# Kernel tuning notes

Measured on AMD Instinct MI355X. Metric: run time of the kernel, lower is better.

The kernel has to match this reference:

```python
import jax, jax.numpy as jnp
import numpy as np

B, N, M = 4, 512, 8192
QUERY_DIM, INPUT_DIM = 512, 256
HEADS, DIM_HEAD = 8, 64
ATT_DIM = HEADS * DIM_HEAD  # 512


def setup_inputs() -> dict:
    key = jax.random.key(0)
    ks = jax.random.split(key, 6)
    x = jax.random.normal(ks[0], (B, N, QUERY_DIM), dtype=jnp.float32)
    context = jax.random.normal(ks[1], (B, M, INPUT_DIM), dtype=jnp.float32)
    # Linear weights stored as [in, out] for x @ W
    Wq = jax.random.normal(ks[2], (QUERY_DIM, ATT_DIM), dtype=jnp.float32) / np.sqrt(QUERY_DIM)
    Wkv = jax.random.normal(ks[3], (INPUT_DIM, 2 * ATT_DIM), dtype=jnp.float32) / np.sqrt(INPUT_DIM)
    Wo = jax.random.normal(ks[4], (ATT_DIM, QUERY_DIM), dtype=jnp.float32) / np.sqrt(ATT_DIM)
    bo = jax.random.normal(ks[5], (QUERY_DIM,), dtype=jnp.float32) * 0.01
    return {"x": x, "context": context, "Wq": Wq, "Wkv": Wkv, "Wo": Wo, "bo": bo}


def reference(x, context, Wq, Wkv, Wo, bo):
    scale = DIM_HEAD ** -0.5
    q = x @ Wq                      # [B, N, H*D]
    kv = context @ Wkv              # [B, M, 2*H*D]
    k, v = jnp.split(kv, 2, axis=-1)
    # split heads: b n (h d) -> b h n d
    q = q.reshape(B, N, HEADS, DIM_HEAD).transpose(0, 2, 1, 3)
    k = k.reshape(B, M, HEADS, DIM_HEAD).transpose(0, 2, 1, 3)
    v = v.reshape(B, M, HEADS, DIM_HEAD).transpose(0, 2, 1, 3)
    scores = jnp.einsum('bhid,bhjd->bhij', q, k) * scale  # [B, H, N, M]
    attn = jax.nn.softmax(scores, axis=-1)
    out = jnp.einsum('bhij,bhjd->bhid', attn, v)           # [B, H, N, D]
    out = out.transpose(0, 2, 1, 3).reshape(B, N, ATT_DIM)
    return out @ Wo + bo
```

## Files before the change

### kernel.cpp

```cpp
#include <hip/hip_runtime.h>
#include <hip/hip_bf16.h>
#include <cstdint>

#define NB 4
#define NQ 512
#define NM 8192
#define NH 8
#define DH 64

typedef short bf16x8s __attribute__((ext_vector_type(8)));
typedef short bf16x4s __attribute__((ext_vector_type(4)));
typedef float f32x4  __attribute__((ext_vector_type(4)));

static __device__ __forceinline__ short f2bs(float f) {
    unsigned u = __builtin_bit_cast(unsigned, f);
    return (short)(unsigned short)((u + 0x8000u) >> 16);
}
static __device__ __forceinline__ unsigned pk2(float a, float b) {
    unsigned au = __builtin_bit_cast(unsigned, a) + 0x8000u;
    unsigned bu = __builtin_bit_cast(unsigned, b) + 0x8000u;
    return __builtin_amdgcn_perm(bu, au, 0x07060302u);
}

#if __has_builtin(__builtin_amdgcn_exp2f)
static __device__ __forceinline__ float fexp2(float x) { return __builtin_amdgcn_exp2f(x); }
#else
static __device__ __forceinline__ float fexp2(float x) { return exp2f(x); }
#endif

__global__ __launch_bounds__(256) void prep_weights(
    const float* __restrict__ Wq, const float* __restrict__ Wo,
    const float* __restrict__ Wkv,
    short* __restrict__ Wqf, short* __restrict__ Wof, short* __restrict__ Wkvf)
{
    const int t = threadIdx.x;
    const int w = t >> 6, ln = t & 63;
    const int m16 = ln & 15, quad = ln >> 4;
    int f = blockIdx.x * 4 + w;
    const float* src; short* dst; int N, KS, n0, ks;
    if (f < 512)       { src = Wq;  dst = Wqf;  N = 512;  KS = 16; n0 = f >> 4; ks = f & 15; }
    else if (f < 1024) { f -= 512;  src = Wo;  dst = Wof;  N = 512;  KS = 16; n0 = f >> 4; ks = f & 15; }
    else               { f -= 1024; src = Wkv; dst = Wkvf; N = 1024; KS = 8;  n0 = f >> 3; ks = f & 7; }
    const float* sp = src + (size_t)(ks * 32 + quad * 8) * N + n0 * 16 + m16;
    float v[8];
    #pragma unroll
    for (int j = 0; j < 8; ++j) v[j] = sp[(size_t)j * N];
    uint4 pkv = { pk2(v[0],v[1]), pk2(v[2],v[3]), pk2(v[4],v[5]), pk2(v[6],v[7]) };
    *(uint4*)(dst + ((size_t)(n0 * KS + ks) * 64 + ln) * 8) = pkv;
}

__device__ __forceinline__ void proj32_body(
    const float* __restrict__ A, const short* __restrict__ Wf,
    float* __restrict__ C, const float* __restrict__ bias,
    int tm, int tn, char* smemraw)
{
    short* As = (short*)smemraw;

    const int t = threadIdx.x;
    const int w = t >> 6, ln = t & 63;
    const int m16 = ln & 15, quad = ln >> 4;
    const int wm = w >> 1, wn = w & 1;

    const int ar = t >> 3, ac = (t & 7) << 3;

    const float* Ap = A + (size_t)(tm * 32 + ar) * 512 + ac;

    f32x4 acc[2] = {};

    for (int k0 = 0; k0 < 512; k0 += 64) {
        float4 a0 = *(const float4*)(Ap + k0);
        float4 a1 = *(const float4*)(Ap + k0 + 4);
        bf16x8s bfr[2][2];
        #pragma unroll
        for (int ks = 0; ks < 2; ++ks)
            #pragma unroll
            for (int nt = 0; nt < 2; ++nt)
                bfr[ks][nt] = *(const bf16x8s*)(Wf +
                    ((size_t)((tn * 4 + wn * 2 + nt) * 16 + (k0 >> 5) + ks) * 64 + ln) * 8);

        __syncthreads();
        {
            uint4 wa = { pk2(a0.x,a0.y), pk2(a0.z,a0.w), pk2(a1.x,a1.y), pk2(a1.z,a1.w) };
            *(uint4*)&As[ar * 72 + ac] = wa;
        }
        __syncthreads();

        #pragma unroll
        for (int ks = 0; ks < 2; ++ks) {
            bf16x8s af = *(const bf16x8s*)&As[(wm * 16 + m16) * 72 + ks * 32 + quad * 8];
            #pragma unroll
            for (int nt = 0; nt < 2; ++nt)
                acc[nt] = __builtin_amdgcn_mfma_f32_16x16x32_bf16(af, bfr[ks][nt], acc[nt], 0, 0, 0);
        }
    }

    const int row0 = tm * 32 + wm * 16 + quad * 4;
    const int col0 = tn * 64 + wn * 32;
    #pragma unroll
    for (int nt = 0; nt < 2; ++nt) {
        const int col = col0 + nt * 16 + m16;
        const float bb = bias ? bias[col] : 0.f;
        #pragma unroll
        for (int r = 0; r < 4; ++r)
            C[(size_t)(row0 + r) * 512 + col] = acc[nt][r] + bb;
    }
}

__device__ __forceinline__ void kv_body(
    const float* __restrict__ A, const short* __restrict__ Wkvf,
    short* __restrict__ Kf, short* __restrict__ Vf,
    int kvid, char* smemraw)
{
    short* As = (short*)smemraw;

    const int t  = threadIdx.x;
    const int tm = ((kvid >> 6) << 3) | (kvid & 7);
    const int tn = (kvid >> 3) & 7;
    const int w  = t >> 6, ln = t & 63;
    const int m16 = ln & 15, quad = ln >> 4;
    const int wm = w & 1, wn = w >> 1;

    const int ar = t >> 3;
    const int ac = (t & 7) << 2;

    const float* Abase = A + (size_t)(tm * 128 + ar) * 256 + ac;

    f32x4 acc[4][4] = {};

    for (int k0 = 0; k0 < 256; k0 += 32) {
        float4 av[4];
        #pragma unroll
        for (int p = 0; p < 4; ++p)
            av[p] = *(const float4*)(Abase + (size_t)p * 32 * 256 + k0);
        bf16x8s bfr[4];
        #pragma unroll
        for (int j = 0; j < 4; ++j)
            bfr[j] = *(const bf16x8s*)(Wkvf +
                ((size_t)((tn * 8 + wn * 4 + j) * 8 + (k0 >> 5)) * 64 + ln) * 8);

        __syncthreads();
        #pragma unroll
        for (int p = 0; p < 4; ++p) {
            uint2 wv = { pk2(av[p].x, av[p].y), pk2(av[p].z, av[p].w) };
            *(uint2*)&As[(p * 32 + ar) * 40 + ac] = wv;
        }
        __syncthreads();

        bf16x8s af[4];
        #pragma unroll
        for (int i = 0; i < 4; ++i)
            af[i] = *(const bf16x8s*)&As[(wm * 64 + i * 16 + m16) * 40 + quad * 8];
        #pragma unroll
        for (int i = 0; i < 4; ++i)
            #pragma unroll
            for (int j = 0; j < 4; ++j)
                acc[i][j] = __builtin_amdgcn_mfma_f32_16x16x32_bf16(af[i], bfr[j], acc[i][j], 0, 0, 0);
    }

    const int col0 = tn * 128 + wn * 64;
    const int row0 = tm * 128 + wm * 64;
    const int b    = row0 >> 13;
    const int mr0  = row0 & (NM - 1);

    if (col0 < 512) {
        const int h = col0 >> 6;
        short* Kp = Kf + (size_t)(b * NH + h) * (NM * DH);
        #pragma unroll
        for (int i = 0; i < 4; ++i)
            #pragma unroll
            for (int j = 0; j < 4; ++j) {
                const int d = j * 16 + m16;
                #pragma unroll
                for (int r = 0; r < 4; ++r) {
                    const int key = mr0 + i * 16 + quad * 4 + r;
                    const int idx = ((key >> 4) * 2 + (d >> 5)) * 512
                                  + (((d >> 3) & 3) * 16 + (key & 15)) * 8 + (d & 7);
                    Kp[idx] = f2bs(acc[i][j][r]);
                }
            }
    } else {
        const int h = (col0 - 512) >> 6;
        short* Vp = Vf + (size_t)(b * NH + h) * (NM * DH);
        #pragma unroll
        for (int j = 0; j < 4; ++j)
            #pragma unroll
            for (int p = 0; p < 2; ++p) {
                uint4 v;
                v.x = pk2(acc[2*p    ][j][0], acc[2*p    ][j][1]);
                v.y = pk2(acc[2*p    ][j][2], acc[2*p    ][j][3]);
                v.z = pk2(acc[2*p + 1][j][0], acc[2*p + 1][j][1]);
                v.w = pk2(acc[2*p + 1][j][2], acc[2*p + 1][j][3]);
                *(uint4*)(Vp + ((size_t)(j * 256 + (mr0 >> 5) + p) * 64 + ln) * 8) = v;
            }
    }
}

__global__ __launch_bounds__(256) void gemm_kvq(
    const float* __restrict__ x,   const short* __restrict__ Wqf, float* __restrict__ q,
    const float* __restrict__ ctx, const short* __restrict__ Wkvf,
    short* __restrict__ Kf, short* __restrict__ Vf)
{
    __shared__ __align__(16) char smem[10240];
    if (blockIdx.x < 512)
        proj32_body(x, Wqf, q, nullptr, (int)(blockIdx.x >> 3), (int)(blockIdx.x & 7), smem);
    else
        kv_body(ctx, Wkvf, Kf, Vf, (int)(blockIdx.x - 512), smem);
}

__global__ __launch_bounds__(256) void gemm_proj32(
    const float* __restrict__ A, const short* __restrict__ Wf,
    float* __restrict__ C, const float* __restrict__ bias)
{
    __shared__ __align__(16) char smem[32 * 72 * 2];
    proj32_body(A, Wf, C, bias, (int)(blockIdx.x >> 3), (int)(blockIdx.x & 7), smem);
}

__global__ __launch_bounds__(512, 2) void attn_mfma(
    const float* __restrict__ Q,
    const short* __restrict__ Kfr,
    const short* __restrict__ Vfr,
    float* __restrict__ Og)
{
    __shared__ __align__(16) float Ob[2][64 * 66];
    __shared__ float lbuf[8 * 64];

    const int bid = blockIdx.x;
    const int xcd = bid & 7, g = bid >> 3;
    const int bh  = xcd * 4 + (g & 3);
    const int qt  = g >> 2;
    const int b   = bh >> 3, h = bh & 7;
    const int t   = threadIdx.x;
    const int w   = t >> 6, ln = t & 63;
    const int m16 = ln & 15, quad = ln >> 4;

    const short* Kbase = Kfr + (size_t)bh * (NM * DH);
    const short* Vbase = Vfr + (size_t)bh * (NM * DH);

    const float qsc = 0.125f * 1.44269504f;
    bf16x8s qf[4][2];
    #pragma unroll
    for (int mt = 0; mt < 4; ++mt) {
        const float* qrow = Q + ((size_t)(b * NQ + qt * 64 + mt * 16 + m16)) * 512 + h * 64;
        #pragma unroll
        for (int ks = 0; ks < 2; ++ks) {
            float4 x0 = *(const float4*)(qrow + ks * 32 + quad * 8);
            float4 x1 = *(const float4*)(qrow + ks * 32 + quad * 8 + 4);
            uint4 pkv = { pk2(x0.x * qsc, x0.y * qsc), pk2(x0.z * qsc, x0.w * qsc),
                          pk2(x1.x * qsc, x1.y * qsc), pk2(x1.z * qsc, x1.w * qsc) };
            qf[mt][ks] = *reinterpret_cast<bf16x8s*>(&pkv);
        }
    }

    bf16x4s ones4;
    #pragma unroll
    for (int j = 0; j < 4; ++j) ones4[j] = (short)0x3F80;

    f32x4 o[4][4] = {};
    f32x4 lsum[4] = {};

    bf16x8s kf[4][2];
    {
        const int kc = w * 64;
        #pragma unroll
        for (int nt = 0; nt < 4; ++nt)
            #pragma unroll
            for (int ks = 0; ks < 2; ++ks)
                kf[nt][ks] = *(const bf16x8s*)(Kbase + ((((kc >> 4) + nt) * 2 + ks) << 9) + ln * 8);
    }

    for (int it = 0; it < 16; ++it) {
        const int kc = it * 512 + w * 64;

        uint4 vraw[4][2];
        #pragma unroll
        for (int dt = 0; dt < 4; ++dt)
            #pragma unroll
            for (int kp = 0; kp < 2; ++kp)
                vraw[dt][kp] = *(const uint4*)(Vbase + ((size_t)(dt * 256 + (kc >> 5) + kp) * 64 + ln) * 8);

        f32x4 st[4][4] = {};
        #pragma unroll
        for (int kt = 0; kt < 4; ++kt)
            #pragma unroll
            for (int mt = 0; mt < 4; ++mt) {
                st[mt][kt] = __builtin_amdgcn_mfma_f32_16x16x32_bf16(kf[kt][0], qf[mt][0], st[mt][kt], 0, 0, 0);
                st[mt][kt] = __builtin_amdgcn_mfma_f32_16x16x32_bf16(kf[kt][1], qf[mt][1], st[mt][kt], 0, 0, 0);
            }

        if (it + 1 < 16) {
            const int kn = (it + 1) * 512 + w * 64;
            #pragma unroll
            for (int nt = 0; nt < 4; ++nt)
                #pragma unroll
                for (int ks = 0; ks < 2; ++ks)
                    kf[nt][ks] = *(const bf16x8s*)(Kbase + ((((kn >> 4) + nt) * 2 + ks) << 9) + ln * 8);
        }

        #pragma unroll
        for (int mt = 0; mt < 4; ++mt)
            #pragma unroll
            for (int kt = 0; kt < 4; ++kt) {
                const float p0 = fexp2(st[mt][kt][0]);
                const float p1 = fexp2(st[mt][kt][1]);
                const float p2 = fexp2(st[mt][kt][2]);
                const float p3 = fexp2(st[mt][kt][3]);
                uint2 pu = { pk2(p0, p1), pk2(p2, p3) };
                bf16x4s pbv = *reinterpret_cast<bf16x4s*>(&pu);
                const int kp = kt >> 1, hh = kt & 1;
                #pragma unroll
                for (int dt = 0; dt < 4; ++dt) {
                    uint2 vh = hh ? make_uint2(vraw[dt][kp].z, vraw[dt][kp].w)
                                  : make_uint2(vraw[dt][kp].x, vraw[dt][kp].y);
                    bf16x4s va = *reinterpret_cast<bf16x4s*>(&vh);
                    o[mt][dt] = __builtin_amdgcn_mfma_f32_16x16x16bf16_1k(va, pbv, o[mt][dt], 0, 0, 0);
                }
                lsum[mt] = __builtin_amdgcn_mfma_f32_16x16x16bf16_1k(ones4, pbv, lsum[mt], 0, 0, 0);
            }
    }

    if (quad == 0) {
        #pragma unroll
        for (int mt = 0; mt < 4; ++mt)
            lbuf[w * 64 + mt * 16 + m16] = lsum[mt][0];
    }
    if (w < 2) {
        float* dst = Ob[w];
        #pragma unroll
        for (int mt = 0; mt < 4; ++mt)
            #pragma unroll
            for (int dt = 0; dt < 4; ++dt)
                *(f32x4*)&dst[(mt * 16 + m16) * 66 + dt * 16 + quad * 4] = o[mt][dt];
    }
    __syncthreads();
    #pragma unroll
    for (int ph = 1; ph < 4; ++ph) {
        if ((w >> 1) == ph) {
            float* dst = Ob[w & 1];
            #pragma unroll
            for (int mt = 0; mt < 4; ++mt)
                #pragma unroll
                for (int dt = 0; dt < 4; ++dt) {
                    float* p = &dst[(mt * 16 + m16) * 66 + dt * 16 + quad * 4];
                    f32x4 cur = *(f32x4*)p;
                    cur += o[mt][dt];
                    *(f32x4*)p = cur;
                }
        }
        __syncthreads();
    }
    {
        const int row = t >> 3;
        const int d0  = (t & 7) << 3;
        float l = 0.f;
        #pragma unroll
        for (int wi = 0; wi < 8; ++wi) l += lbuf[wi * 64 + row];
        const float inv = 1.0f / l;
        float* op = Og + ((size_t)(b * NQ + qt * 64 + row)) * 512 + h * 64 + d0;
        #pragma unroll
        for (int j = 0; j < 2; ++j) {
            const int c = row * 66 + d0 + j * 4;
            float4 r;
            r.x = (Ob[0][c + 0] + Ob[1][c + 0]) * inv;
            r.y = (Ob[0][c + 1] + Ob[1][c + 1]) * inv;
            r.z = (Ob[0][c + 2] + Ob[1][c + 2]) * inv;
            r.w = (Ob[0][c + 3] + Ob[1][c + 3]) * inv;
            *(float4*)(op + j * 4) = r;
        }
    }
}

extern "C" void kernel_launch(void* const* d_in, const int* in_sizes, int n_in,
                              void* d_out, int out_size, void* d_ws, size_t ws_size,
                              hipStream_t stream) {
    (void)in_sizes; (void)n_in; (void)out_size; (void)ws_size;

    const float* x   = (const float*)d_in[0];
    const float* ctx = (const float*)d_in[1];
    const float* Wq  = (const float*)d_in[2];
    const float* Wkv = (const float*)d_in[3];
    const float* Wo  = (const float*)d_in[4];
    const float* bo  = (const float*)d_in[5];
    float* out = (float*)d_out;

    float* ws    = (float*)d_ws;
    float* q     = ws;
    float* attno = q + (size_t)2048 * 512;
    short* Kf    = (short*)(attno + (size_t)2048 * 512);
    short* Vf    = Kf + (size_t)NB * NH * NM * DH;
    short* Wqf   = Vf + (size_t)NB * NH * NM * DH;
    short* Wof   = Wqf + (size_t)512 * 512;
    short* Wkvf  = Wof + (size_t)512 * 512;

    prep_weights<<<dim3(384), dim3(256), 0, stream>>>(Wq, Wo, Wkv, Wqf, Wof, Wkvf);

    gemm_kvq<<<dim3(2560), dim3(256), 0, stream>>>(x, Wqf, q, ctx, Wkvf, Kf, Vf);

    attn_mfma<<<dim3(256), dim3(512), 0, stream>>>(q, Kf, Vf, attno);

    gemm_proj32<<<dim3(512), dim3(256), 0, stream>>>(attno, Wof, out, bo);
}
```

Baseline: 188.6 us.

## Double-buffer LDS A tiles in projection GEMMs with one barrier per step

The Q and KV projection GEMM bodies now keep two LDS buffers for the bf16-converted A tile. Each step prefetches the next global A slice into registers, runs the MFMAs on the current buffer, then writes the next buffer, so only one barrier is needed per k-step instead of two. This is meant to hide global load latency behind the MFMAs, at the cost of doubled shared memory and more registers, which may reduce occupancy.

```diff
diff --git a/kernel.cpp b/kernel.cpp
--- a/kernel.cpp
+++ b/kernel.cpp
@@ -67,9 +67,18 @@
 
     f32x4 acc[2] = {};
 
+    {
+        float4 a0 = *(const float4*)(Ap);
+        float4 a1 = *(const float4*)(Ap + 4);
+        uint4 wa = { pk2(a0.x,a0.y), pk2(a0.z,a0.w), pk2(a1.x,a1.y), pk2(a1.z,a1.w) };
+        *(uint4*)&As[ar * 72 + ac] = wa;
+    }
+
+    #pragma unroll
     for (int k0 = 0; k0 < 512; k0 += 64) {
-        float4 a0 = *(const float4*)(Ap + k0);
-        float4 a1 = *(const float4*)(Ap + k0 + 4);
+        short* Ab = As + ((k0 >> 6) & 1) * 2304;
+        __syncthreads();
+
         bf16x8s bfr[2][2];
         #pragma unroll
         for (int ks = 0; ks < 2; ++ks)
@@ -78,19 +87,27 @@
                 bfr[ks][nt] = *(const bf16x8s*)(Wf +
                     ((size_t)((tn * 4 + wn * 2 + nt) * 16 + (k0 >> 5) + ks) * 64 + ln) * 8);
 
-        __syncthreads();
-        {
-            uint4 wa = { pk2(a0.x,a0.y), pk2(a0.z,a0.w), pk2(a1.x,a1.y), pk2(a1.z,a1.w) };
-            *(uint4*)&As[ar * 72 + ac] = wa;
-        }
-        __syncthreads();
-
-        #pragma unroll
-        for (int ks = 0; ks < 2; ++ks) {
-            bf16x8s af = *(const bf16x8s*)&As[(wm * 16 + m16) * 72 + ks * 32 + quad * 8];
+        bf16x8s afr[2];
+        #pragma unroll
+        for (int ks = 0; ks < 2; ++ks)
+            afr[ks] = *(const bf16x8s*)&Ab[(wm * 16 + m16) * 72 + ks * 32 + quad * 8];
+
+        float4 a0n, a1n;
+        if (k0 + 64 < 512) {
+            a0n = *(const float4*)(Ap + k0 + 64);
+            a1n = *(const float4*)(Ap + k0 + 68);
+        }
+
+        #pragma unroll
+        for (int ks = 0; ks < 2; ++ks)
             #pragma unroll
             for (int nt = 0; nt < 2; ++nt)
-                acc[nt] = __builtin_amdgcn_mfma_f32_16x16x32_bf16(af, bfr[ks][nt], acc[nt], 0, 0, 0);
+                acc[nt] = __builtin_amdgcn_mfma_f32_16x16x32_bf16(afr[ks], bfr[ks][nt], acc[nt], 0, 0, 0);
+
+        if (k0 + 64 < 512) {
+            short* Abn = As + ((((k0 >> 6) + 1) & 1)) * 2304;
+            uint4 wa = { pk2(a0n.x,a0n.y), pk2(a0n.z,a0n.w), pk2(a1n.x,a1n.y), pk2(a1n.z,a1n.w) };
+            *(uint4*)&Abn[ar * 72 + ac] = wa;
         }
     }
 
@@ -127,34 +144,55 @@
 
     f32x4 acc[4][4] = {};
 
+    {
+        float4 av[4];
+        #pragma unroll
+        for (int p = 0; p < 4; ++p)
+            av[p] = *(const float4*)(Abase + (size_t)p * 32 * 256);
+        #pragma unroll
+        for (int p = 0; p < 4; ++p) {
+            uint2 wv = { pk2(av[p].x, av[p].y), pk2(av[p].z, av[p].w) };
+            *(uint2*)&As[(p * 32 + ar) * 40 + ac] = wv;
+        }
+    }
+
+    #pragma unroll
     for (int k0 = 0; k0 < 256; k0 += 32) {
-        float4 av[4];
-        #pragma unroll
-        for (int p = 0; p < 4; ++p)
-            av[p] = *(const float4*)(Abase + (size_t)p * 32 * 256 + k0);
+        short* Ab = As + ((k0 >> 5) & 1) * 5120;
+        __syncthreads();
+
         bf16x8s bfr[4];
         #pragma unroll
         for (int j = 0; j < 4; ++j)
             bfr[j] = *(const bf16x8s*)(Wkvf +
                 ((size_t)((tn * 8 + wn * 4 + j) * 8 + (k0 >> 5)) * 64 + ln) * 8);
 
-        __syncthreads();
-        #pragma unroll
-        for (int p = 0; p < 4; ++p) {
-            uint2 wv = { pk2(av[p].x, av[p].y), pk2(av[p].z, av[p].w) };
-            *(uint2*)&As[(p * 32 + ar) * 40 + ac] = wv;
-        }
-        __syncthreads();
-
         bf16x8s af[4];
         #pragma unroll
         for (int i = 0; i < 4; ++i)
-            af[i] = *(const bf16x8s*)&As[(wm * 64 + i * 16 + m16) * 40 + quad * 8];
+            af[i] = *(const bf16x8s*)&Ab[(wm * 64 + i * 16 + m16) * 40 + quad * 8];
+
+        float4 avn[4];
+        if (k0 + 32 < 256) {
+            #pragma unroll
+            for (int p = 0; p < 4; ++p)
+                avn[p] = *(const float4*)(Abase + (size_t)p * 32 * 256 + k0 + 32);
+        }
+
         #pragma unroll
         for (int i = 0; i < 4; ++i)
             #pragma unroll
             for (int j = 0; j < 4; ++j)
                 acc[i][j] = __builtin_amdgcn_mfma_f32_16x16x32_bf16(af[i], bfr[j], acc[i][j], 0, 0, 0);
+
+        if (k0 + 32 < 256) {
+            short* Abn = As + (((k0 >> 5) + 1) & 1) * 5120;
+            #pragma unroll
+            for (int p = 0; p < 4; ++p) {
+                uint2 wv = { pk2(avn[p].x, avn[p].y), pk2(avn[p].z, avn[p].w) };
+                *(uint2*)&Abn[(p * 32 + ar) * 40 + ac] = wv;
+            }
+        }
     }
 
     const int col0 = tn * 128 + wn * 64;
@@ -200,7 +238,7 @@
     const float* __restrict__ ctx, const short* __restrict__ Wkvf,
     short* __restrict__ Kf, short* __restrict__ Vf)
 {
-    __shared__ __align__(16) char smem[10240];
+    __shared__ __align__(16) char smem[20480];
     if (blockIdx.x < 512)
         proj32_body(x, Wqf, q, nullptr, (int)(blockIdx.x >> 3), (int)(blockIdx.x & 7), smem);
     else
@@ -211,7 +249,7 @@
     const float* __restrict__ A, const short* __restrict__ Wf,
     float* __restrict__ C, const float* __restrict__ bias)
 {
-    __shared__ __align__(16) char smem[32 * 72 * 2];
+    __shared__ __align__(16) char smem[32 * 72 * 2 * 2];
     proj32_body(A, Wf, C, bias, (int)(blockIdx.x >> 3), (int)(blockIdx.x & 7), smem);
 }
 
```

Result: no change. 187.5 us (-0.5%).
